# Optimization experiments

Measured on AMD Instinct MI355X. Metric: run time of the kernel, lower is better.

## Reference

```python
import jax, jax.numpy as jnp
import numpy as np

N = 10000      # nodes of this type
T = 160000     # total metapath instances (ragged rows)
D = 256        # input_dim
P = 256        # pre_embed_dim
H = 512        # mlp_settings['layer_list'][0]
S = 64         # select_dim


def setup_inputs() -> dict:
    key = jax.random.key(0)
    ks = jax.random.split(key, 16)
    def w(k, shape):
        return jax.random.normal(k, shape, jnp.float32) / np.sqrt(shape[0]).astype(np.float32)
    return {
        "feat_A": jax.random.normal(ks[0], (N, D), jnp.float32),
        "feat_AP": jax.random.normal(ks[1], (T, D), jnp.float32),
        "feat_APA": jax.random.normal(ks[2], (T, 2 * D), jnp.float32),
        "seg_AP": jnp.sort(jax.random.randint(ks[3], (T,), 0, N, jnp.int32)),
        "seg_APA": jnp.sort(jax.random.randint(ks[4], (T,), 0, N, jnp.int32)),
        "type_weight": w(ks[5], (D, P)),
        "W_enc_AP": w(ks[6], (D, H)),   "b_enc_AP": jnp.zeros((H,), jnp.float32),
        "W_dec_AP": w(ks[7], (H, P)),   "b_dec_AP": jnp.zeros((P,), jnp.float32),
        "W_enc_APA": w(ks[8], (2 * D, H)), "b_enc_APA": jnp.zeros((H,), jnp.float32),
        "W_dec_APA": w(ks[9], (H, P)),  "b_dec_APA": jnp.zeros((P,), jnp.float32),
        "W_attn1": w(ks[10], (2 * P, 2 * P)),
        "W_attn2": w(ks[11], (2 * P, 1)),
        "W_cls": w(ks[12], (P, S)), "b_cls": jnp.zeros((S,), jnp.float32),
    }


def reference(feat_A, feat_AP, feat_APA, seg_AP, seg_APA, type_weight,
              W_enc_AP, b_enc_AP, W_dec_AP, b_dec_AP,
              W_enc_APA, b_enc_APA, W_dec_APA, b_dec_APA,
              W_attn1, W_attn2, W_cls, b_cls):
    # center node embedding (metapath of length 1): feat @ type_weight
    center = feat_A @ type_weight                                  # [N, P]

    def metapath_path(feat, seg, We, be, Wd, bd):
        # per-metapath MLP encode (Linear+ReLU) / decode (Linear)
        h = jax.nn.relu(feat @ We + be)                            # [T, H]
        dec = h @ Wd + bd                                          # [T, P]
        # ragged split + per-node sum aggregation; empty segments -> zeros
        return jax.ops.segment_sum(dec, seg, num_segments=N,
                                   indices_are_sorted=True)        # [N, P]

    inj_AP = metapath_path(feat_AP, seg_AP, W_enc_AP, b_enc_AP, W_dec_AP, b_dec_AP)
    inj_APA = metapath_path(feat_APA, seg_APA, W_enc_APA, b_enc_APA, W_dec_APA, b_dec_APA)

    def attn_score(inj):
        # attn = Tanh -> Linear(2P,2P,no bias) -> Linear(2P,1,no bias) -> LeakyReLU(0.1), then mean
        x = jnp.tanh(jnp.concatenate([center, inj], axis=1))       # [N, 2P]
        s = (x @ W_attn1) @ W_attn2                                # [N, 1]
        return jax.nn.leaky_relu(s, 0.1).mean()

    # index 0 corresponds to the length-1 metapath (never scored; fixed to 0)
    scores = jnp.stack([jnp.zeros((), jnp.float32), attn_score(inj_AP), attn_score(inj_APA)])
    wts = jax.nn.softmax(scores)                                   # [3]

    inj_AP = inj_AP * wts[1]
    inj_APA = inj_APA * wts[2]
    embed = (inj_AP + inj_APA) * 0.5                               # stack(...,dim=2).mean(dim=2)
    pre_embed = jax.nn.log_softmax((center + embed) @ W_cls + b_cls, axis=1)  # [N, S]
    return pre_embed, inj_AP, inj_APA
```

## Files before the change

kernel.cpp:

```cpp
#include <hip/hip_runtime.h>
#include <stdint.h>

typedef __bf16 bf16x8 __attribute__((ext_vector_type(8)));
typedef __bf16 bf16x4 __attribute__((ext_vector_type(4)));
typedef float  f32x4  __attribute__((ext_vector_type(4)));

#define N_NODES 10000
#define T_ROWS  160000
#define HDIM    512
#define PDIM    256
#define NCTILES 157

__device__ __forceinline__ f32x4 mfma16(bf16x8 a, bf16x8 b, f32x4 c) {
    return __builtin_amdgcn_mfma_f32_16x16x32_bf16(a, b, c, 0, 0, 0);
}

__device__ __forceinline__ void pack_one(const float* __restrict__ W,
                                         __bf16* __restrict__ out,
                                         int K, int Nc, int ltid) {
    int lane = ltid & 63;
    int t = ltid >> 6;
    int KT = K >> 5;
    int kt = t % KT, nt = t / KT;
    int col = (nt << 4) + (lane & 15);
    int krow = (kt << 5) + ((lane >> 4) << 3);
    __bf16* dst = out + ((size_t)ltid << 3);
#pragma unroll
    for (int e = 0; e < 8; ++e)
        dst[e] = (__bf16)W[(size_t)(krow + e) * Nc + col];
}

__global__ void pack6_kernel(
    const float* __restrict__ tw,    __bf16* __restrict__ twP,
    const float* __restrict__ WeAP,  __bf16* __restrict__ WeAPp,
    const float* __restrict__ WdAP,  __bf16* __restrict__ WdAPp,
    const float* __restrict__ WeAPA, __bf16* __restrict__ WeAPAp,
    const float* __restrict__ WdAPA, __bf16* __restrict__ WdAPAp,
    const float* __restrict__ W1, const float* __restrict__ W2,
    float* __restrict__ vbuf)
{
    int tid = blockIdx.x * 512 + threadIdx.x;
    if      (tid <  8192) pack_one(tw,    twP,    256, 256, tid);
    else if (tid < 24576) pack_one(WeAP,  WeAPp,  256, 512, tid - 8192);
    else if (tid < 40960) pack_one(WdAP,  WdAPp,  512, 256, tid - 24576);
    else if (tid < 73728) pack_one(WeAPA, WeAPAp, 512, 512, tid - 40960);
    else if (tid < 90112) pack_one(WdAPA, WdAPAp, 512, 256, tid - 73728);
    else if (tid < 90624) {
        int k = tid - 90112;
        float s = 0.f;
        for (int j = 0; j < 512; ++j) s += W1[k * 512 + j] * W2[j];
        vbuf[k] = s;
    }
}

template<int DIN>
__device__ __forceinline__ void path_body(
    const float* __restrict__ X,
    const __bf16* __restrict__ WeP, const float* __restrict__ be,
    const __bf16* __restrict__ WdP, const float* __restrict__ bd,
    const int* __restrict__ seg,
    float* __restrict__ inj,
    int tile, __bf16* buf, int* segs)
{
    constexpr int LDX = DIN + 8;
    constexpr int LDH = HDIM + 8;
    constexpr int LDP = 260;
    constexpr int KT1 = DIN / 32;
    const int tid = threadIdx.x;
    const int row0 = tile * 64;
    if (tid < 64) segs[tid] = seg[row0 + tid];

#pragma unroll 4
    for (int i = tid; i < 64 * (DIN / 4); i += 512) {
        int r = i / (DIN / 4), c4 = i % (DIN / 4);
        float4 f = ((const float4*)X)[(size_t)(row0 + r) * (DIN / 4) + c4];
        bf16x4 h;
        h[0] = (__bf16)f.x; h[1] = (__bf16)f.y; h[2] = (__bf16)f.z; h[3] = (__bf16)f.w;
        *(bf16x4*)&buf[r * LDX + c4 * 4] = h;
    }
    __syncthreads();

    const int wave = tid >> 6, lane = tid & 63;
    const int lr = lane & 15, lg = lane >> 4;

    f32x4 acc1[4][4] = {};
    {
        const __bf16* w1 = WeP + ((size_t)(wave * 4) * KT1) * 512 + lane * 8;
        bf16x8 bX[4], bY[4], a[4];
#pragma unroll
        for (int ht = 0; ht < 4; ++ht) bX[ht] = *(const bf16x8*)&w1[(size_t)(ht * KT1) * 512];
        for (int kt = 0; kt < KT1; kt += 2) {
#pragma unroll
            for (int ht = 0; ht < 4; ++ht)
                bY[ht] = *(const bf16x8*)&w1[(size_t)(ht * KT1 + kt + 1) * 512];
            int ko = kt * 32 + lg * 8;
#pragma unroll
            for (int xt = 0; xt < 4; ++xt)
                a[xt] = *(const bf16x8*)&buf[(xt * 16 + lr) * LDX + ko];
            __builtin_amdgcn_s_setprio(1);
#pragma unroll
            for (int ht = 0; ht < 4; ++ht)
#pragma unroll
                for (int xt = 0; xt < 4; ++xt)
                    acc1[ht][xt] = mfma16(bX[ht], a[xt], acc1[ht][xt]);
            __builtin_amdgcn_s_setprio(0);
            int kn = (kt + 2 < KT1) ? kt + 2 : 0;
#pragma unroll
            for (int ht = 0; ht < 4; ++ht)
                bX[ht] = *(const bf16x8*)&w1[(size_t)(ht * KT1 + kn) * 512];
            ko = (kt + 1) * 32 + lg * 8;
#pragma unroll
            for (int xt = 0; xt < 4; ++xt)
                a[xt] = *(const bf16x8*)&buf[(xt * 16 + lr) * LDX + ko];
            __builtin_amdgcn_s_setprio(1);
#pragma unroll
            for (int ht = 0; ht < 4; ++ht)
#pragma unroll
                for (int xt = 0; xt < 4; ++xt)
                    acc1[ht][xt] = mfma16(bY[ht], a[xt], acc1[ht][xt]);
            __builtin_amdgcn_s_setprio(0);
        }
    }
    __syncthreads();

#pragma unroll
    for (int ht = 0; ht < 4; ++ht) {
        int hcol0 = wave * 64 + ht * 16 + lg * 4;
        f32x4 bias = *(const f32x4*)&be[hcol0];
#pragma unroll
        for (int xt = 0; xt < 4; ++xt) {
            int xrow = xt * 16 + lr;
            bf16x4 hv;
#pragma unroll
            for (int j = 0; j < 4; ++j) {
                float vl = acc1[ht][xt][j] + bias[j];
                hv[j] = (__bf16)(vl > 0.f ? vl : 0.f);
            }
            *(bf16x4*)&buf[xrow * LDH + hcol0] = hv;
        }
    }
    __syncthreads();

    f32x4 acc2[4][2] = {};
    {
        const __bf16* w2 = WdP + ((size_t)(wave * 2) * 16) * 512 + lane * 8;
        bf16x8 bX2[2], bY2[2], aX[4], aY[4];
#pragma unroll
        for (int ct = 0; ct < 2; ++ct) bX2[ct] = *(const bf16x8*)&w2[(size_t)(ct * 16) * 512];
#pragma unroll
        for (int rt = 0; rt < 4; ++rt)
            aX[rt] = *(const bf16x8*)&buf[(rt * 16 + lr) * LDH + lg * 8];
        for (int kt = 0; kt < 16; kt += 2) {
#pragma unroll
            for (int ct = 0; ct < 2; ++ct)
                bY2[ct] = *(const bf16x8*)&w2[(size_t)(ct * 16 + kt + 1) * 512];
            int ko = (kt + 1) * 32 + lg * 8;
#pragma unroll
            for (int rt = 0; rt < 4; ++rt)
                aY[rt] = *(const bf16x8*)&buf[(rt * 16 + lr) * LDH + ko];
            __builtin_amdgcn_s_setprio(1);
#pragma unroll
            for (int ct = 0; ct < 2; ++ct)
#pragma unroll
                for (int rt = 0; rt < 4; ++rt)
                    acc2[rt][ct] = mfma16(aX[rt], bX2[ct], acc2[rt][ct]);
            __builtin_amdgcn_s_setprio(0);
            int kn = (kt + 2 < 16) ? kt + 2 : 0;
#pragma unroll
            for (int ct = 0; ct < 2; ++ct)
                bX2[ct] = *(const bf16x8*)&w2[(size_t)(ct * 16 + kn) * 512];
            ko = kn * 32 + lg * 8;
#pragma unroll
            for (int rt = 0; rt < 4; ++rt)
                aX[rt] = *(const bf16x8*)&buf[(rt * 16 + lr) * LDH + ko];
            __builtin_amdgcn_s_setprio(1);
#pragma unroll
            for (int ct = 0; ct < 2; ++ct)
#pragma unroll
                for (int rt = 0; rt < 4; ++rt)
                    acc2[rt][ct] = mfma16(aY[rt], bY2[ct], acc2[rt][ct]);
            __builtin_amdgcn_s_setprio(0);
        }
    }
    __syncthreads();

    float* decs = (float*)buf;
#pragma unroll
    for (int ct = 0; ct < 2; ++ct) {
        int col = wave * 32 + ct * 16 + lr;
        float bias = bd[col];
#pragma unroll
        for (int rt = 0; rt < 4; ++rt) {
            int rbase = rt * 16 + lg * 4;
#pragma unroll
            for (int j = 0; j < 4; ++j)
                decs[(rbase + j) * LDP + col] = acc2[rt][ct][j] + bias;
        }
    }

    {
        const int c  = wave * 32 + (lane & 31);
        const int rs = (lane >> 5) * 32;
        float run = decs[rs * LDP + c];
        int cur = segs[rs];
        int runstart = rs;
#pragma unroll
        for (int r = rs + 1; r < rs + 32; ++r) {
            int s = segs[r];
            float v = decs[r * LDP + c];
            if (s == cur) run += v;
            else {
                if (runstart != rs) inj[(size_t)cur * PDIM + c] = run;
                else atomicAdd(&inj[(size_t)cur * PDIM + c], run);
                cur = s; run = v; runstart = r;
            }
        }
        atomicAdd(&inj[(size_t)cur * PDIM + c], run);
    }
}

__device__ __forceinline__ void center_body(
    const float* __restrict__ feat, const __bf16* __restrict__ twP,
    float* __restrict__ center, int tile, __bf16* xs)
{
    constexpr int LDX = 264;
    const int tid = threadIdx.x;
    const int row0 = tile * 64;
#pragma unroll 4
    for (int i = tid; i < 64 * 64; i += 512) {
        int r = i / 64, c4 = i % 64;
        int row = row0 + r;
        float4 f = {0.f, 0.f, 0.f, 0.f};
        if (row < N_NODES) f = ((const float4*)feat)[(size_t)row * 64 + c4];
        bf16x4 h;
        h[0] = (__bf16)f.x; h[1] = (__bf16)f.y; h[2] = (__bf16)f.z; h[3] = (__bf16)f.w;
        *(bf16x4*)&xs[r * LDX + c4 * 4] = h;
    }
    __syncthreads();

    const int wave = tid >> 6, lane = tid & 63;
    const int lr = lane & 15, lg = lane >> 4;
    f32x4 acc[4][2] = {};
    const __bf16* w = twP + ((size_t)(wave * 2) * 8) * 512 + lane * 8;
    for (int kt = 0; kt < 8; ++kt) {
        int ko = kt * 32 + lg * 8;
        bf16x8 a[4];
#pragma unroll
        for (int rt = 0; rt < 4; ++rt)
            a[rt] = *(const bf16x8*)&xs[(rt * 16 + lr) * LDX + ko];
#pragma unroll
        for (int ct = 0; ct < 2; ++ct) {
            bf16x8 b = *(const bf16x8*)&w[(size_t)(ct * 8 + kt) * 512];
#pragma unroll
            for (int rt = 0; rt < 4; ++rt)
                acc[rt][ct] = mfma16(a[rt], b, acc[rt][ct]);
        }
    }
#pragma unroll
    for (int ct = 0; ct < 2; ++ct) {
        int col = wave * 32 + ct * 16 + lr;
#pragma unroll
        for (int rt = 0; rt < 4; ++rt) {
            int rbase = rt * 16 + lg * 4;
#pragma unroll
            for (int j = 0; j < 4; ++j) {
                int row = row0 + rbase + j;
                if (row < N_NODES) center[(size_t)row * 256 + col] = acc[rt][ct][j];
            }
        }
    }
}

__global__ __launch_bounds__(512, 4) void paths_kernel(
    const float* __restrict__ featAP,  const float* __restrict__ featAPA,
    const __bf16* __restrict__ WeAPp,  const float* __restrict__ beAP,
    const __bf16* __restrict__ WdAPp,  const float* __restrict__ bdAP,
    const __bf16* __restrict__ WeAPAp, const float* __restrict__ beAPA,
    const __bf16* __restrict__ WdAPAp, const float* __restrict__ bdAPA,
    const int* __restrict__ segAP, const int* __restrict__ segAPA,
    float* __restrict__ injAP, float* __restrict__ injAPA,
    const float* __restrict__ featA, const __bf16* __restrict__ twP,
    float* __restrict__ center)
{
    __shared__ __bf16 buf[64 * (HDIM + 8)];
    __shared__ int segs[64];
    int bid = blockIdx.x;
    if (bid < NCTILES) {
        center_body(featA, twP, center, bid, buf);
        return;
    }
    int p = bid - NCTILES;
    int tile = p >> 1;
    if (p & 1)
        path_body<512>(featAPA, WeAPAp, beAPA, WdAPAp, bdAPA, segAPA, injAPA,
                       tile, buf, segs);
    else
        path_body<256>(featAP, WeAPp, beAP, WdAPp, bdAP, segAP, injAP,
                       tile, buf, segs);
}

__global__ __launch_bounds__(256, 4) void score2_kernel(
    const float* __restrict__ center, const float* __restrict__ injAP,
    const float* __restrict__ injAPA, const float* __restrict__ v,
    float* __restrict__ sacc)
{
    const int w = threadIdx.x >> 6, lane = threadIdx.x & 63;
    float l1 = 0.f, l2 = 0.f;
    for (int row = blockIdx.x * 4 + w; row < N_NODES; row += gridDim.x * 4) {
        float x1 = 0.f, x2 = 0.f;
#pragma unroll
        for (int k = 0; k < 4; ++k) {
            int c = lane + k * 64;
            size_t off = (size_t)row * 256 + c;
            float tc = tanhf(center[off]) * v[c];
            float vi = v[256 + c];
            x1 += tc + tanhf(injAP[off]) * vi;
            x2 += tc + tanhf(injAPA[off]) * vi;
        }
#pragma unroll
        for (int o = 32; o > 0; o >>= 1) {
            x1 += __shfl_xor(x1, o);
            x2 += __shfl_xor(x2, o);
        }
        if (lane == 0) {
            l1 += (x1 > 0.f) ? x1 : 0.1f * x1;
            l2 += (x2 > 0.f) ? x2 : 0.1f * x2;
        }
    }
    if (lane == 0) {
        atomicAdd(&sacc[0], l1);
        atomicAdd(&sacc[1], l2);
    }
}

__global__ __launch_bounds__(256, 4) void final_kernel(
    const float* __restrict__ center, const float* __restrict__ injAP,
    const float* __restrict__ injAPA, const float* __restrict__ sacc,
    const float* __restrict__ Wcls, const float* __restrict__ bcls,
    float* __restrict__ out0, float* __restrict__ out1, float* __restrict__ out2)
{
    __shared__ float zs[4][256];
    float s1 = sacc[0] * (1.f / N_NODES), s2 = sacc[1] * (1.f / N_NODES);
    float m0 = fmaxf(0.f, fmaxf(s1, s2));
    float e0 = expf(0.f - m0), e1 = expf(s1 - m0), e2 = expf(s2 - m0);
    float inv = 1.f / (e0 + e1 + e2);
    const float w1 = e1 * inv, w2 = e2 * inv;

    const int row0 = blockIdx.x * 4;
    for (int idx = threadIdx.x; idx < 1024; idx += 256) {
        int r = idx >> 8, c = idx & 255;
        size_t off = (size_t)(row0 + r) * 256 + c;
        float a = injAP[off] * w1, b = injAPA[off] * w2;
        out1[off] = a; out2[off] = b;
        zs[r][c] = center[off] + 0.5f * (a + b);
    }
    __syncthreads();
    const int g = threadIdx.x >> 6, j = threadIdx.x & 63;
    float logit = bcls[j];
    for (int k = 0; k < 256; ++k) logit += zs[g][k] * Wcls[k * 64 + j];
    float m = logit;
#pragma unroll
    for (int o = 32; o > 0; o >>= 1) m = fmaxf(m, __shfl_xor(m, o));
    float e = expf(logit - m);
    float se = e;
#pragma unroll
    for (int o = 32; o > 0; o >>= 1) se += __shfl_xor(se, o);
    out0[(size_t)(row0 + g) * 64 + j] = (logit - m) - logf(se);
}

extern "C" void kernel_launch(void* const* d_in, const int* in_sizes, int n_in,
                              void* d_out, int out_size, void* d_ws, size_t ws_size,
                              hipStream_t stream)
{
    const float* feat_A   = (const float*)d_in[0];
    const float* feat_AP  = (const float*)d_in[1];
    const float* feat_APA = (const float*)d_in[2];
    const int*   seg_AP   = (const int*)d_in[3];
    const int*   seg_APA  = (const int*)d_in[4];
    const float* type_w   = (const float*)d_in[5];
    const float* We_AP    = (const float*)d_in[6];
    const float* be_AP    = (const float*)d_in[7];
    const float* Wd_AP    = (const float*)d_in[8];
    const float* bd_AP    = (const float*)d_in[9];
    const float* We_APA   = (const float*)d_in[10];
    const float* be_APA   = (const float*)d_in[11];
    const float* Wd_APA   = (const float*)d_in[12];
    const float* bd_APA   = (const float*)d_in[13];
    const float* W_attn1  = (const float*)d_in[14];
    const float* W_attn2  = (const float*)d_in[15];
    const float* W_cls    = (const float*)d_in[16];
    const float* b_cls    = (const float*)d_in[17];

    char* ws = (char*)d_ws;
    size_t o = 0;
    auto alloc = [&](size_t bytes) { char* p = ws + o; o += (bytes + 255) & ~size_t(255); return p; };
    float* center = (float*)alloc((size_t)N_NODES * 256 * 4);
    float* injAP  = (float*)alloc((size_t)N_NODES * 256 * 4);
    float* injAPA = (float*)alloc((size_t)N_NODES * 256 * 4);
    float* vbuf   = (float*)alloc(512 * 4);
    float* sacc   = (float*)alloc(256);
    __bf16* twP    = (__bf16*)alloc(256 * 256 * 2);
    __bf16* WeAPp  = (__bf16*)alloc(256 * 512 * 2);
    __bf16* WdAPp  = (__bf16*)alloc(512 * 256 * 2);
    __bf16* WeAPAp = (__bf16*)alloc(512 * 512 * 2);
    __bf16* WdAPAp = (__bf16*)alloc(512 * 256 * 2);

    hipMemsetAsync(injAP,  0, (size_t)N_NODES * 256 * 4, stream);
    hipMemsetAsync(injAPA, 0, (size_t)N_NODES * 256 * 4, stream);
    hipMemsetAsync(sacc,   0, 256, stream);

    pack6_kernel<<<177, 512, 0, stream>>>(type_w, twP, We_AP, WeAPp, Wd_AP, WdAPp,
                                          We_APA, WeAPAp, Wd_APA, WdAPAp,
                                          W_attn1, W_attn2, vbuf);
    paths_kernel<<<NCTILES + 2 * (T_ROWS / 64), 512, 0, stream>>>(
        feat_AP, feat_APA, WeAPp, be_AP, WdAPp, bd_AP,
        WeAPAp, be_APA, WdAPAp, bd_APA, seg_AP, seg_APA, injAP, injAPA,
        feat_A, twP, center);
    score2_kernel<<<256, 256, 0, stream>>>(center, injAP, injAPA, vbuf, sacc);

    float* out0 = (float*)d_out;
    float* out1 = out0 + (size_t)N_NODES * 64;
    float* out2 = out1 + (size_t)N_NODES * 256;
    final_kernel<<<N_NODES / 4, 256, 0, stream>>>(center, injAP, injAPA, sacc,
                                                  W_cls, b_cls, out0, out1, out2);
}
```

Measured before the change: 422.9 us.

## Stream input features through double-buffered LDS slices during encoder GEMM

Instead of loading and converting the whole 64-row input tile into shared memory before the first GEMM, each thread now prefetches one 32-column k-slice per iteration into registers and writes it to a small double-buffered LDS slot. Global loads of X overlap with MFMA work on the previous slice. The operand order is also swapped so the accumulators map rows-by-columns, which changes the hidden-layer writeback to scalar bf16 stores. The cost is a __syncthreads per k-step, and the scalar stores may cause LDS bank conflicts.

```diff
diff --git a/kernel.cpp b/kernel.cpp
--- a/kernel.cpp
+++ b/kernel.cpp
@@ -60,83 +60,76 @@
     const __bf16* __restrict__ WdP, const float* __restrict__ bd,
     const int* __restrict__ seg,
     float* __restrict__ inj,
-    int tile, __bf16* buf, int* segs)
-{
-    constexpr int LDX = DIN + 8;
+    int tile, __bf16* bufh, __bf16* xbuf, int* segs)
+{
     constexpr int LDH = HDIM + 8;
     constexpr int LDP = 260;
     constexpr int KT1 = DIN / 32;
+    constexpr int LDK = 36;
+    constexpr int SLOT = 64 * LDK;
     const int tid = threadIdx.x;
     const int row0 = tile * 64;
     if (tid < 64) segs[tid] = seg[row0 + tid];
 
-#pragma unroll 4
-    for (int i = tid; i < 64 * (DIN / 4); i += 512) {
-        int r = i / (DIN / 4), c4 = i % (DIN / 4);
-        float4 f = ((const float4*)X)[(size_t)(row0 + r) * (DIN / 4) + c4];
-        bf16x4 h;
-        h[0] = (__bf16)f.x; h[1] = (__bf16)f.y; h[2] = (__bf16)f.z; h[3] = (__bf16)f.w;
-        *(bf16x4*)&buf[r * LDX + c4 * 4] = h;
-    }
-    __syncthreads();
+    const int xr = tid >> 3, xc = tid & 7;
+    const float4* Xrow = (const float4*)X + (size_t)(row0 + xr) * (DIN / 4) + xc;
 
     const int wave = tid >> 6, lane = tid & 63;
     const int lr = lane & 15, lg = lane >> 4;
+
+    float4 xhold, xf;
+    {
+        float4 x0 = Xrow[0];
+        bf16x4 h; h[0] = (__bf16)x0.x; h[1] = (__bf16)x0.y;
+        h[2] = (__bf16)x0.z; h[3] = (__bf16)x0.w;
+        *(bf16x4*)&xbuf[xr * LDK + xc * 4] = h;
+    }
+    xhold = Xrow[8];
+    __syncthreads();
 
     f32x4 acc1[4][4] = {};
     {
         const __bf16* w1 = WeP + ((size_t)(wave * 4) * KT1) * 512 + lane * 8;
-        bf16x8 bX[4], bY[4], a[4];
-#pragma unroll
-        for (int ht = 0; ht < 4; ++ht) bX[ht] = *(const bf16x8*)&w1[(size_t)(ht * KT1) * 512];
-        for (int kt = 0; kt < KT1; kt += 2) {
-#pragma unroll
-            for (int ht = 0; ht < 4; ++ht)
-                bY[ht] = *(const bf16x8*)&w1[(size_t)(ht * KT1 + kt + 1) * 512];
-            int ko = kt * 32 + lg * 8;
-#pragma unroll
-            for (int xt = 0; xt < 4; ++xt)
-                a[xt] = *(const bf16x8*)&buf[(xt * 16 + lr) * LDX + ko];
+#pragma unroll 2
+        for (int kt = 0; kt < KT1; ++kt) {
+            const int s = kt & 1;
+            if (kt + 2 < KT1) xf = Xrow[(kt + 2) * 8];
+            if (kt + 1 < KT1) {
+                bf16x4 h; h[0] = (__bf16)xhold.x; h[1] = (__bf16)xhold.y;
+                h[2] = (__bf16)xhold.z; h[3] = (__bf16)xhold.w;
+                *(bf16x4*)&xbuf[(s ^ 1) * SLOT + xr * LDK + xc * 4] = h;
+            }
+            bf16x8 b[4], a[4];
+#pragma unroll
+            for (int ct = 0; ct < 4; ++ct)
+                b[ct] = *(const bf16x8*)&w1[(size_t)(ct * KT1 + kt) * 512];
+#pragma unroll
+            for (int rt = 0; rt < 4; ++rt)
+                a[rt] = *(const bf16x8*)&xbuf[s * SLOT + (rt * 16 + lr) * LDK + lg * 8];
             __builtin_amdgcn_s_setprio(1);
 #pragma unroll
-            for (int ht = 0; ht < 4; ++ht)
-#pragma unroll
-                for (int xt = 0; xt < 4; ++xt)
-                    acc1[ht][xt] = mfma16(bX[ht], a[xt], acc1[ht][xt]);
+            for (int ct = 0; ct < 4; ++ct)
+#pragma unroll
+                for (int rt = 0; rt < 4; ++rt)
+                    acc1[rt][ct] = mfma16(a[rt], b[ct], acc1[rt][ct]);
             __builtin_amdgcn_s_setprio(0);
-            int kn = (kt + 2 < KT1) ? kt + 2 : 0;
-#pragma unroll
-            for (int ht = 0; ht < 4; ++ht)
-                bX[ht] = *(const bf16x8*)&w1[(size_t)(ht * KT1 + kn) * 512];
-            ko = (kt + 1) * 32 + lg * 8;
-#pragma unroll
-            for (int xt = 0; xt < 4; ++xt)
-                a[xt] = *(const bf16x8*)&buf[(xt * 16 + lr) * LDX + ko];
-            __builtin_amdgcn_s_setprio(1);
-#pragma unroll
-            for (int ht = 0; ht < 4; ++ht)
-#pragma unroll
-                for (int xt = 0; xt < 4; ++xt)
-                    acc1[ht][xt] = mfma16(bY[ht], a[xt], acc1[ht][xt]);
-            __builtin_amdgcn_s_setprio(0);
-        }
-    }
-    __syncthreads();
-
-#pragma unroll
-    for (int ht = 0; ht < 4; ++ht) {
-        int hcol0 = wave * 64 + ht * 16 + lg * 4;
-        f32x4 bias = *(const f32x4*)&be[hcol0];
-#pragma unroll
-        for (int xt = 0; xt < 4; ++xt) {
-            int xrow = xt * 16 + lr;
-            bf16x4 hv;
+            __syncthreads();
+            xhold = xf;
+        }
+    }
+
+#pragma unroll
+    for (int ct = 0; ct < 4; ++ct) {
+        int col = wave * 64 + ct * 16 + lr;
+        float bias = be[col];
+#pragma unroll
+        for (int rt = 0; rt < 4; ++rt) {
+            int rbase = rt * 16 + lg * 4;
 #pragma unroll
             for (int j = 0; j < 4; ++j) {
-                float vl = acc1[ht][xt][j] + bias[j];
-                hv[j] = (__bf16)(vl > 0.f ? vl : 0.f);
+                float vl = acc1[rt][ct][j] + bias;
+                bufh[(rbase + j) * LDH + col] = (__bf16)(vl > 0.f ? vl : 0.f);
             }
-            *(bf16x4*)&buf[xrow * LDH + hcol0] = hv;
         }
     }
     __syncthreads();
@@ -149,7 +142,7 @@
         for (int ct = 0; ct < 2; ++ct) bX2[ct] = *(const bf16x8*)&w2[(size_t)(ct * 16) * 512];
 #pragma unroll
         for (int rt = 0; rt < 4; ++rt)
-            aX[rt] = *(const bf16x8*)&buf[(rt * 16 + lr) * LDH + lg * 8];
+            aX[rt] = *(const bf16x8*)&bufh[(rt * 16 + lr) * LDH + lg * 8];
         for (int kt = 0; kt < 16; kt += 2) {
 #pragma unroll
             for (int ct = 0; ct < 2; ++ct)
@@ -157,7 +150,7 @@
             int ko = (kt + 1) * 32 + lg * 8;
 #pragma unroll
             for (int rt = 0; rt < 4; ++rt)
-                aY[rt] = *(const bf16x8*)&buf[(rt * 16 + lr) * LDH + ko];
+                aY[rt] = *(const bf16x8*)&bufh[(rt * 16 + lr) * LDH + ko];
             __builtin_amdgcn_s_setprio(1);
 #pragma unroll
             for (int ct = 0; ct < 2; ++ct)
@@ -172,7 +165,7 @@
             ko = kn * 32 + lg * 8;
 #pragma unroll
             for (int rt = 0; rt < 4; ++rt)
-                aX[rt] = *(const bf16x8*)&buf[(rt * 16 + lr) * LDH + ko];
+                aX[rt] = *(const bf16x8*)&bufh[(rt * 16 + lr) * LDH + ko];
             __builtin_amdgcn_s_setprio(1);
 #pragma unroll
             for (int ct = 0; ct < 2; ++ct)
@@ -184,7 +177,7 @@
     }
     __syncthreads();
 
-    float* decs = (float*)buf;
+    float* decs = (float*)bufh;
 #pragma unroll
     for (int ct = 0; ct < 2; ++ct) {
         int col = wave * 32 + ct * 16 + lr;
@@ -282,21 +275,22 @@
     const float* __restrict__ featA, const __bf16* __restrict__ twP,
     float* __restrict__ center)
 {
-    __shared__ __bf16 buf[64 * (HDIM + 8)];
+    __shared__ __bf16 bufh[64 * (HDIM + 8)];
+    __shared__ __bf16 xbuf[2 * 64 * 36];
     __shared__ int segs[64];
     int bid = blockIdx.x;
     if (bid < NCTILES) {
-        center_body(featA, twP, center, bid, buf);
+        center_body(featA, twP, center, bid, bufh);
         return;
     }
     int p = bid - NCTILES;
     int tile = p >> 1;
     if (p & 1)
         path_body<512>(featAPA, WeAPAp, beAPA, WdAPAp, bdAPA, segAPA, injAPA,
-                       tile, buf, segs);
+                       tile, bufh, xbuf, segs);
     else
         path_body<256>(featAP, WeAPp, beAP, WdAPp, bdAP, segAP, injAP,
-                       tile, buf, segs);
+                       tile, bufh, xbuf, segs);
 }
 
 __global__ __launch_bounds__(256, 4) void score2_kernel(
```

After: 556.5 us. +31.6%, slower.
